# Kernel tuning notes

Hardware: AMD Instinct MI355X
Metric: run time of the kernel (lower is better)

The kernel has to match this reference:

```python
import jax, jax.numpy as jnp
import numpy as np

N_NODES = 100000


def _gcn_conv(x, W, b, src, dst, norm, num_nodes):
    # PyG GCNConv: h = x @ W; out = scatter_add(norm_e * h[src] -> dst) + b
    h = x @ W                               # [N, out]
    msgs = h[src] * norm[:, None]           # [E', out]
    agg = jax.ops.segment_sum(msgs, dst, num_segments=num_nodes)
    return agg + b


def _gcn_norm(edge_index, num_nodes):
    # add self-loops, then sym-normalize: deg^-1/2[src] * deg^-1/2[dst]
    loops = jnp.arange(num_nodes, dtype=edge_index.dtype)
    src = jnp.concatenate([edge_index[0], loops])
    dst = jnp.concatenate([edge_index[1], loops])
    deg = jax.ops.segment_sum(jnp.ones_like(dst, dtype=jnp.float32), dst,
                              num_segments=num_nodes)
    dis = jnp.where(deg > 0, jax.lax.rsqrt(jnp.maximum(deg, 1.0)), 0.0)
    norm = dis[src] * dis[dst]              # [E + N]
    return src, dst, norm


def setup_inputs() -> dict:
    key = jax.random.key(0)
    k1, k2, k3, k4 = jax.random.split(key, 4)
    in_feat, hidden, n_classes = 512, 16, 16
    n_edges = 3200000
    x = jax.random.normal(k1, (N_NODES, in_feat), dtype=jnp.float32)
    edge_index = jax.random.randint(k2, (2, n_edges), 0, N_NODES, dtype=jnp.int64)
    W1 = jax.random.normal(k3, (in_feat, hidden), dtype=jnp.float32) / np.sqrt(in_feat)
    b1 = jnp.zeros((hidden,), dtype=jnp.float32)
    W2 = jax.random.normal(k4, (hidden, n_classes), dtype=jnp.float32) / np.sqrt(hidden)
    b2 = jnp.zeros((n_classes,), dtype=jnp.float32)
    return {"x": x, "edge_index": edge_index, "W1": W1, "b1": b1, "W2": W2, "b2": b2}


def reference(x, edge_index, W1, b1, W2, b2):
    num_nodes = x.shape[0]
    src, dst, norm = _gcn_norm(edge_index, num_nodes)
    h = _gcn_conv(x, W1, b1, src, dst, norm, num_nodes)
    h = jax.nn.relu(h)
    # dropout is identity at inference (training=False)
    h = _gcn_conv(h, W2, b2, src, dst, norm, num_nodes)
    return jax.nn.log_softmax(h, axis=1)
```

## Files before the change

### kernel.cpp

```cpp
#include <hip/hip_runtime.h>
#include <hip/hip_bf16.h>
#include <math.h>

#define NNODES 100000
#define NBUCK 8
#define XRANGE 12500
#define NCHUNK 32
#define CAP 408192
#define BCHUNK 3125
#define GT64 1563

typedef __attribute__((ext_vector_type(8))) short bf16x8;
typedef __attribute__((ext_vector_type(4))) float f32x4;

__device__ __forceinline__ float bflo(unsigned int u) {
  union { unsigned int i; float f; } v; v.i = u << 16; return v.f;
}
__device__ __forceinline__ float bfhi(unsigned int u) {
  union { unsigned int i; float f; } v; v.i = u & 0xFFFF0000u; return v.f;
}
__device__ __forceinline__ unsigned int f2bf1(float f) {
  union { float f; unsigned int i; } v; v.f = f;
  return (v.i + 0x7FFFu + ((v.i >> 16) & 1u)) >> 16;
}
__device__ __forceinline__ unsigned int f2bf2(float a, float b) {
  return f2bf1(a) | (f2bf1(b) << 16);
}

__device__ __forceinline__ int edge_val(const void* eidx, int is64, size_t i) {
  if (is64) return (int)((const long long*)eidx)[i];
  return ((const int*)eidx)[i];
}

__device__ __forceinline__ bf16x8 cvt8(const float4& p, const float4& q) {
  union { unsigned int u[4]; bf16x8 v; } r;
  r.u[0] = f2bf2(p.x, p.y);
  r.u[1] = f2bf2(p.z, p.w);
  r.u[2] = f2bf2(q.x, q.y);
  r.u[3] = f2bf2(q.z, q.w);
  return r.v;
}

__device__ __forceinline__ bf16x8 cvtW(const float* wf) {
  union { unsigned int u[4]; bf16x8 v; } r;
  r.u[0] = f2bf2(wf[0], wf[1]);
  r.u[1] = f2bf2(wf[2], wf[3]);
  r.u[2] = f2bf2(wf[4], wf[5]);
  r.u[3] = f2bf2(wf[6], wf[7]);
  return r.v;
}

__global__ void k_init(const void* eidx, int* flag, int* gcur) {
  int t = threadIdx.x;
  int bad = 0;
  const unsigned long long* p = (const unsigned long long*)eidx;
  for (int i = t; i < 1024; i += 64)
    if (p[i] >> 32) bad = 1;
  unsigned long long b = __ballot(bad);
  if (t == 0) flag[0] = (b == 0ULL) ? 1 : 0;
  if (t < NBUCK) gcur[t] = 0;
}

__global__ void k_binmm(const void* eidx, const int* __restrict__ flag, int* gcur,
                        int* __restrict__ sArr, unsigned short* __restrict__ dArr,
                        int E, int binBlocks,
                        const float* __restrict__ x, const float* __restrict__ W,
                        unsigned short* __restrict__ gb, int gemmBlocks) {
  __shared__ unsigned int s_sb[BCHUNK];
  __shared__ unsigned short s_dl[BCHUNK];
  __shared__ int bbase[NBUCK], lcur[NBUCK], wcnt[4][NBUCK];

  int grp = blockIdx.x / 11, role = blockIdx.x % 11;
  if (role < 3) {
    int gid = grp * 3 + role;
    if (gid >= gemmBlocks) return;
    int wid = threadIdx.x >> 6;
    int tile = gid * 4 + wid;
    if (tile >= GT64) return;
    int lane = threadIdx.x & 63;
    int row0 = tile * 64;
    int q8 = lane >> 4;
    int jm = lane & 15;
    const float4* x4 = (const float4*)x;
    size_t xb0 = (size_t)min(row0 + jm,      NNODES - 1) * 128 + q8 * 2;
    size_t xb1 = (size_t)min(row0 + 16 + jm, NNODES - 1) * 128 + q8 * 2;
    size_t xb2 = (size_t)min(row0 + 32 + jm, NNODES - 1) * 128 + q8 * 2;
    size_t xb3 = (size_t)min(row0 + 48 + jm, NNODES - 1) * 128 + q8 * 2;

    f32x4 acc0 = {0.f, 0.f, 0.f, 0.f}, acc1 = {0.f, 0.f, 0.f, 0.f};
    f32x4 acc2 = {0.f, 0.f, 0.f, 0.f}, acc3 = {0.f, 0.f, 0.f, 0.f};
    #pragma unroll
    for (int kc = 0; kc < 16; ++kc) {
      float4 va0 = x4[xb0 + kc * 8], va1 = x4[xb0 + kc * 8 + 1];
      float4 vb0 = x4[xb1 + kc * 8], vb1 = x4[xb1 + kc * 8 + 1];
      float4 vc0 = x4[xb2 + kc * 8], vc1 = x4[xb2 + kc * 8 + 1];
      float4 vd0 = x4[xb3 + kc * 8], vd1 = x4[xb3 + kc * 8 + 1];
      float wf[8];
      #pragma unroll
      for (int i = 0; i < 8; ++i)
        wf[i] = W[(size_t)(kc * 32 + q8 * 8 + i) * 16 + jm];
      bf16x8 bfr = cvtW(wf);
      acc0 = __builtin_amdgcn_mfma_f32_16x16x32_bf16(cvt8(va0, va1), bfr, acc0, 0, 0, 0);
      acc1 = __builtin_amdgcn_mfma_f32_16x16x32_bf16(cvt8(vb0, vb1), bfr, acc1, 0, 0, 0);
      acc2 = __builtin_amdgcn_mfma_f32_16x16x32_bf16(cvt8(vc0, vc1), bfr, acc2, 0, 0, 0);
      acc3 = __builtin_amdgcn_mfma_f32_16x16x32_bf16(cvt8(vd0, vd1), bfr, acc3, 0, 0, 0);
    }
    #pragma unroll
    for (int r = 0; r < 4; ++r) {
      int rl = q8 * 4 + r;
      int w0 = row0 + rl, w1 = row0 + 16 + rl, w2 = row0 + 32 + rl, w3 = row0 + 48 + rl;
      if (w0 < NNODES) gb[(size_t)w0 * 16 + jm] = (unsigned short)f2bf1(acc0[r]);
      if (w1 < NNODES) gb[(size_t)w1 * 16 + jm] = (unsigned short)f2bf1(acc1[r]);
      if (w2 < NNODES) gb[(size_t)w2 * 16 + jm] = (unsigned short)f2bf1(acc2[r]);
      if (w3 < NNODES) gb[(size_t)w3 * 16 + jm] = (unsigned short)f2bf1(acc3[r]);
    }
    return;
  }

  int bid = grp * 8 + (role - 3);
  if (bid >= binBlocks) return;
  int is64 = flag[0];
  int beg = bid * BCHUNK;
  int end = min(beg + BCHUNK, E);
  int cnt = end - beg;
  int lane = threadIdx.x & 63, wid = threadIdx.x >> 6;

  int cl = 0;
  for (int i = threadIdx.x; i < cnt; i += 256) {
    int e = beg + i;
    int s = edge_val(eidx, is64, e);
    int d = edge_val(eidx, is64, (size_t)E + e);
    int bk = d / XRANGE;
    s_sb[i] = (unsigned int)s | ((unsigned int)bk << 17);
    s_dl[i] = (unsigned short)(d - bk * XRANGE);
    #pragma unroll
    for (int b = 0; b < NBUCK; ++b) {
      unsigned long long m = __ballot(bk == b);
      if (lane == b) cl += __popcll(m);
    }
  }
  if (lane < NBUCK) wcnt[wid][lane] = cl;
  __syncthreads();
  if (threadIdx.x < NBUCK) {
    int t = wcnt[0][threadIdx.x] + wcnt[1][threadIdx.x] +
            wcnt[2][threadIdx.x] + wcnt[3][threadIdx.x];
    bbase[threadIdx.x] = atomicAdd(&gcur[threadIdx.x], t);
    lcur[threadIdx.x] = 0;
  }
  __syncthreads();

  for (int i = threadIdx.x; i < cnt; i += 256) {
    unsigned int sb = s_sb[i];
    int bk = (int)(sb >> 17);
    int s = (int)(sb & 0x1FFFFu);
    unsigned short dl = s_dl[i];
    #pragma unroll
    for (int b = 0; b < NBUCK; ++b) {
      unsigned long long m = __ballot(bk == b);
      int c = __popcll(m);
      if (!c) continue;
      int leader = __ffsll((unsigned long long)m) - 1;
      int base = 0;
      if (lane == leader) base = atomicAdd(&lcur[b], c);
      base = __shfl(base, leader);
      if (bk == b) {
        int rank = __popcll(m & ((1ULL << lane) - 1));
        int gpos = bbase[b] + base + rank;
        if (gpos < CAP) {
          sArr[(size_t)b * CAP + gpos] = s;
          dArr[(size_t)b * CAP + gpos] = dl;
        }
      }
    }
  }
}

__global__ void k_hist(const int* __restrict__ gcur, const unsigned short* __restrict__ dArr,
                       int* __restrict__ cntc) {
  int b = blockIdx.x & (NBUCK - 1);
  int c = blockIdx.x >> 3;
  __shared__ int h[XRANGE];
  for (int i = threadIdx.x; i < XRANGE; i += 256) h[i] = 0;
  __syncthreads();
  int nE = min(gcur[b], CAP);
  int ce = (nE + NCHUNK - 1) / NCHUNK;
  int beg = c * ce, end = min(beg + ce, nE);
  const unsigned short* dp = dArr + (size_t)b * CAP;
  for (int e = beg + threadIdx.x; e < end; e += 256)
    atomicAdd(&h[dp[e]], 1);
  __syncthreads();
  int lo = b * XRANGE;
  for (int i = threadIdx.x; i < XRANGE; i += 256)
    cntc[(size_t)c * NNODES + lo + i] = h[i];
}

__global__ void k_dis(const int* __restrict__ cntc, int* __restrict__ tot,
                      float* __restrict__ dis, int* __restrict__ bsum,
                      unsigned int* __restrict__ gb1, int n) {
  int i = blockIdx.x * 256 + threadIdx.x;
  int t = 0;
  if (i < n) {
    #pragma unroll
    for (int c = 0; c < NCHUNK; ++c) t += cntc[(size_t)c * NNODES + i];
    tot[i] = t;
    float dd = rsqrtf((float)(t + 1));
    dis[i] = dd;
    uint4* g4 = (uint4*)gb1;
    uint4 pa = g4[(size_t)i * 2], pb = g4[(size_t)i * 2 + 1];
    pa.x = f2bf2(bflo(pa.x) * dd, bfhi(pa.x) * dd);
    pa.y = f2bf2(bflo(pa.y) * dd, bfhi(pa.y) * dd);
    pa.z = f2bf2(bflo(pa.z) * dd, bfhi(pa.z) * dd);
    pa.w = f2bf2(bflo(pa.w) * dd, bfhi(pa.w) * dd);
    pb.x = f2bf2(bflo(pb.x) * dd, bfhi(pb.x) * dd);
    pb.y = f2bf2(bflo(pb.y) * dd, bfhi(pb.y) * dd);
    pb.z = f2bf2(bflo(pb.z) * dd, bfhi(pb.z) * dd);
    pb.w = f2bf2(bflo(pb.w) * dd, bfhi(pb.w) * dd);
    g4[(size_t)i * 2] = pa;
    g4[(size_t)i * 2 + 1] = pb;
  }
  int v = t;
  #pragma unroll
  for (int d = 32; d > 0; d >>= 1) v += __shfl_down(v, d);
  __shared__ int ws4[4];
  if ((threadIdx.x & 63) == 0) ws4[threadIdx.x >> 6] = v;
  __syncthreads();
  if (threadIdx.x == 0) bsum[blockIdx.x] = ws4[0] + ws4[1] + ws4[2] + ws4[3];
}

__global__ void k_scan_fc(const int* __restrict__ tot, const int* __restrict__ bsum,
                          int* __restrict__ rowptr, int* __restrict__ cntc, int n, int nb) {
  __shared__ int ps[512];
  __shared__ int s[256];
  int t = threadIdx.x;
  ps[t] = (t < nb) ? bsum[t] : 0;
  ps[t + 256] = (t + 256 < nb) ? bsum[t + 256] : 0;
  __syncthreads();
  for (int d = 1; d < 512; d <<= 1) {
    int u0 = (t >= d) ? ps[t - d] : 0;
    int u1 = (t + 256 >= d) ? ps[t + 256 - d] : 0;
    __syncthreads();
    ps[t] += u0;
    ps[t + 256] += u1;
    __syncthreads();
  }
  int bex = (blockIdx.x == 0) ? 0 : ps[blockIdx.x - 1];
  if (blockIdx.x == 0 && t == 0) rowptr[n] = ps[nb - 1];

  int idx = blockIdx.x * 256 + t;
  int v = (idx < n) ? tot[idx] : 0;
  s[t] = v;
  __syncthreads();
  for (int d = 1; d < 256; d <<= 1) {
    int u = (t >= d) ? s[t - d] : 0;
    __syncthreads();
    s[t] += u;
    __syncthreads();
  }
  if (idx < n) {
    int run = bex + s[t] - v;
    rowptr[idx] = run;
    #pragma unroll
    for (int c = 0; c < NCHUNK; ++c) {
      size_t id2 = (size_t)c * NNODES + idx;
      int tc = cntc[id2];
      cntc[id2] = run;
      run += tc;
    }
  }
}

__global__ void k_scatter(const int* __restrict__ gcur, const int* __restrict__ sArr,
                          const unsigned short* __restrict__ dArr,
                          const int* __restrict__ cntc, int* __restrict__ col) {
  int b = blockIdx.x & (NBUCK - 1);
  int c = blockIdx.x >> 3;
  __shared__ int cur[XRANGE];
  int lo = b * XRANGE;
  for (int i = threadIdx.x; i < XRANGE; i += 256)
    cur[i] = cntc[(size_t)c * NNODES + lo + i];
  __syncthreads();
  int nE = min(gcur[b], CAP);
  int ce = (nE + NCHUNK - 1) / NCHUNK;
  int beg = c * ce, end = min(beg + ce, nE);
  const int* sp = sArr + (size_t)b * CAP;
  const unsigned short* dp = dArr + (size_t)b * CAP;
  for (int e = beg + threadIdx.x; e < end; e += 256) {
    int d = dp[e];
    int pos = atomicAdd(&cur[d], 1);
    col[pos] = sp[e];
  }
}

__global__ void k_gemm2(const float* __restrict__ o1, const float* __restrict__ W,
                        const float* __restrict__ dis, unsigned int* __restrict__ gb, int nrows) {
  int row = blockIdx.x * blockDim.x + threadIdx.x;
  if (row >= nrows) return;
  const float4* xr = (const float4*)(o1 + (size_t)row * 16);
  float4 x0 = xr[0], x1 = xr[1], x2 = xr[2], x3 = xr[3];
  float xv[16] = {x0.x, x0.y, x0.z, x0.w, x1.x, x1.y, x1.z, x1.w,
                  x2.x, x2.y, x2.z, x2.w, x3.x, x3.y, x3.z, x3.w};
  float acc[16];
  #pragma unroll
  for (int j = 0; j < 16; ++j) acc[j] = 0.f;
  #pragma unroll
  for (int k = 0; k < 16; ++k) {
    const float* wr = W + (size_t)k * 16;
    #pragma unroll
    for (int j = 0; j < 16; ++j)
      acc[j] = fmaf(xv[k], wr[j], acc[j]);
  }
  float dd = dis[row];
  uint4 pa, pb;
  pa.x = f2bf2(acc[0] * dd, acc[1] * dd);
  pa.y = f2bf2(acc[2] * dd, acc[3] * dd);
  pa.z = f2bf2(acc[4] * dd, acc[5] * dd);
  pa.w = f2bf2(acc[6] * dd, acc[7] * dd);
  pb.x = f2bf2(acc[8] * dd, acc[9] * dd);
  pb.y = f2bf2(acc[10] * dd, acc[11] * dd);
  pb.z = f2bf2(acc[12] * dd, acc[13] * dd);
  pb.w = f2bf2(acc[14] * dd, acc[15] * dd);
  uint4* g4 = (uint4*)gb;
  g4[(size_t)row * 2] = pa;
  g4[(size_t)row * 2 + 1] = pb;
}

__device__ __forceinline__ void gather8v2(const uint4* gp, const int* __restrict__ col,
                                          int beg, int end, int h, int slot, float* acc) {
  #pragma unroll
  for (int j = 0; j < 8; ++j) acc[j] = 0.f;
  for (int e = beg + slot; e < end; e += 16) {
    int s = col[e];
    uint4 v = gp[(size_t)s * 2 + h];
    acc[0] += bflo(v.x); acc[1] += bfhi(v.x);
    acc[2] += bflo(v.y); acc[3] += bfhi(v.y);
    acc[4] += bflo(v.z); acc[5] += bfhi(v.z);
    acc[6] += bflo(v.w); acc[7] += bfhi(v.w);
  }
  #pragma unroll
  for (int d = 2; d < 32; d <<= 1) {
    #pragma unroll
    for (int j = 0; j < 8; ++j) acc[j] += __shfl_xor(acc[j], d);
  }
}

__global__ void k_agg1(const unsigned int* __restrict__ gb, const int* __restrict__ col,
                       const int* __restrict__ rowptr, const float* __restrict__ dis,
                       const float* __restrict__ bias, float* __restrict__ o1) {
  int wid = threadIdx.x >> 6;
  int lane = threadIdx.x & 63;
  int n2 = lane >> 5;
  int node = blockIdx.x * 8 + wid * 2 + n2;
  if (node >= NNODES) return;
  int rem = lane & 31;
  int h = rem & 1, slot = rem >> 1;
  const uint4* gp = (const uint4*)gb;
  float acc[8];
  gather8v2(gp, col, rowptr[node], rowptr[node + 1], h, slot, acc);
  uint4 sv = gp[(size_t)node * 2 + h];
  acc[0] += bflo(sv.x); acc[1] += bfhi(sv.x);
  acc[2] += bflo(sv.y); acc[3] += bfhi(sv.y);
  acc[4] += bflo(sv.z); acc[5] += bfhi(sv.z);
  acc[6] += bflo(sv.w); acc[7] += bfhi(sv.w);
  float dd = dis[node];
  const float4* b4 = (const float4*)bias;
  float4 ba = b4[2 * h], bb = b4[2 * h + 1];
  float z0 = fmaxf(fmaf(dd, acc[0], ba.x), 0.f);
  float z1 = fmaxf(fmaf(dd, acc[1], ba.y), 0.f);
  float z2 = fmaxf(fmaf(dd, acc[2], ba.z), 0.f);
  float z3 = fmaxf(fmaf(dd, acc[3], ba.w), 0.f);
  float z4 = fmaxf(fmaf(dd, acc[4], bb.x), 0.f);
  float z5 = fmaxf(fmaf(dd, acc[5], bb.y), 0.f);
  float z6 = fmaxf(fmaf(dd, acc[6], bb.z), 0.f);
  float z7 = fmaxf(fmaf(dd, acc[7], bb.w), 0.f);
  if (slot == 0) {
    float4* o4 = (float4*)o1;
    o4[(size_t)node * 4 + 2 * h] = make_float4(z0, z1, z2, z3);
    o4[(size_t)node * 4 + 2 * h + 1] = make_float4(z4, z5, z6, z7);
  }
}

__global__ void k_agg2(const unsigned int* __restrict__ gb, const int* __restrict__ col,
                       const int* __restrict__ rowptr, const float* __restrict__ dis,
                       const float* __restrict__ bias, float* __restrict__ out) {
  int wid = threadIdx.x >> 6;
  int lane = threadIdx.x & 63;
  int n2 = lane >> 5;
  int node = blockIdx.x * 8 + wid * 2 + n2;
  if (node >= NNODES) return;
  int rem = lane & 31;
  int h = rem & 1, slot = rem >> 1;
  const uint4* gp = (const uint4*)gb;
  float acc[8];
  gather8v2(gp, col, rowptr[node], rowptr[node + 1], h, slot, acc);
  uint4 sv = gp[(size_t)node * 2 + h];
  acc[0] += bflo(sv.x); acc[1] += bfhi(sv.x);
  acc[2] += bflo(sv.y); acc[3] += bfhi(sv.y);
  acc[4] += bflo(sv.z); acc[5] += bfhi(sv.z);
  acc[6] += bflo(sv.w); acc[7] += bfhi(sv.w);
  float dd = dis[node];
  const float4* b4 = (const float4*)bias;
  float4 ba = b4[2 * h], bb = b4[2 * h + 1];
  float z[8];
  z[0] = fmaf(dd, acc[0], ba.x); z[1] = fmaf(dd, acc[1], ba.y);
  z[2] = fmaf(dd, acc[2], ba.z); z[3] = fmaf(dd, acc[3], ba.w);
  z[4] = fmaf(dd, acc[4], bb.x); z[5] = fmaf(dd, acc[5], bb.y);
  z[6] = fmaf(dd, acc[6], bb.z); z[7] = fmaf(dd, acc[7], bb.w);
  float m = z[0];
  #pragma unroll
  for (int j = 1; j < 8; ++j) m = fmaxf(m, z[j]);
  m = fmaxf(m, __shfl_xor(m, 1));
  float se = 0.f;
  #pragma unroll
  for (int j = 0; j < 8; ++j) se += expf(z[j] - m);
  se += __shfl_xor(se, 1);
  float lg = m + logf(se);
  if (slot == 0) {
    float4* o4 = (float4*)out;
    o4[(size_t)node * 4 + 2 * h] = make_float4(z[0] - lg, z[1] - lg, z[2] - lg, z[3] - lg);
    o4[(size_t)node * 4 + 2 * h + 1] = make_float4(z[4] - lg, z[5] - lg, z[6] - lg, z[7] - lg);
  }
}

extern "C" void kernel_launch(void* const* d_in, const int* in_sizes, int n_in,
                              void* d_out, int out_size, void* d_ws, size_t ws_size,
                              hipStream_t stream) {
  const float* x  = (const float*)d_in[0];
  const void*  ei = d_in[1];
  const float* W1 = (const float*)d_in[2];
  const float* b1 = (const float*)d_in[3];
  const float* W2 = (const float*)d_in[4];
  const float* b2 = (const float*)d_in[5];
  float* out = (float*)d_out;

  const int n = NNODES;
  const int E = in_sizes[1] / 2;

  char* ws = (char*)d_ws;
  size_t off = 0;
  auto alloc = [&](size_t bytes) -> void* {
    void* p = ws + off;
    off = (off + bytes + 255) & ~(size_t)255;
    return p;
  };
  int*            flag   = (int*)            alloc(256);
  int*            gcur   = (int*)            alloc(256);
  int*            sArr   = (int*)            alloc((size_t)NBUCK * CAP * 4);
  unsigned short* dArr   = (unsigned short*) alloc((size_t)NBUCK * CAP * 2);
  int*            cntc   = (int*)            alloc((size_t)NCHUNK * n * 4);
  int*            tot    = (int*)            alloc((size_t)n * 4);
  float*          dis    = (float*)          alloc((size_t)n * 4);
  int*            rowptr = (int*)            alloc((size_t)(n + 1) * 4);
  int*            bsum   = (int*)            alloc(4096);
  int*            col    = (int*)            alloc((size_t)E * 4);
  unsigned short* gb1    = (unsigned short*) alloc((size_t)n * 16 * 2);
  float*          o1  = (float*)sArr;
  unsigned int*   gb2 = (unsigned int*)dArr;
  (void)ws_size; (void)n_in; (void)out_size;

  int nb = (n + 255) / 256;
  int binBlocks  = (E + BCHUNK - 1) / BCHUNK;
  int gemmBlocks = (GT64 + 3) / 4;
  int groups = max((gemmBlocks + 2) / 3, (binBlocks + 7) / 8);
  int grid = groups * 11;

  k_init<<<1, 64, 0, stream>>>(ei, flag, gcur);
  k_binmm<<<grid, 256, 0, stream>>>(ei, flag, gcur, sArr, dArr, E, binBlocks,
                                    x, W1, gb1, gemmBlocks);
  k_hist<<<NBUCK * NCHUNK, 256, 0, stream>>>(gcur, dArr, cntc);
  k_dis<<<nb, 256, 0, stream>>>(cntc, tot, dis, bsum, (unsigned int*)gb1, n);
  k_scan_fc<<<nb, 256, 0, stream>>>(tot, bsum, rowptr, cntc, n, nb);
  k_scatter<<<NBUCK * NCHUNK, 256, 0, stream>>>(gcur, sArr, dArr, cntc, col);

  k_agg1<<<(n + 7) / 8, 256, 0, stream>>>((const unsigned int*)gb1, col, rowptr, dis, b1, o1);
  k_gemm2<<<(n + 255) / 256, 256, 0, stream>>>(o1, W2, dis, (unsigned int*)gb2, n);
  k_agg2<<<(n + 7) / 8, 256, 0, stream>>>(gb2, col, rowptr, dis, b2, out);
}
```

Measured before the change: 198.5 us.

## Spread first-layer GEMM tiles across binning, histogram, degree and scan kernels

```diff
diff --git a/kernel.cpp b/kernel.cpp
--- a/kernel.cpp
+++ b/kernel.cpp
@@ -48,6 +48,50 @@
   r.u[2] = f2bf2(wf[4], wf[5]);
   r.u[3] = f2bf2(wf[6], wf[7]);
   return r.v;
+}
+
+__device__ __forceinline__ void gemm_tile64(const float* __restrict__ x,
+                                            const float* __restrict__ W,
+                                            unsigned short* __restrict__ gb,
+                                            int tile) {
+  if (tile >= GT64) return;
+  int lane = threadIdx.x & 63;
+  int row0 = tile * 64;
+  int q8 = lane >> 4;
+  int jm = lane & 15;
+  const float4* x4 = (const float4*)x;
+  size_t xb0 = (size_t)min(row0 + jm,      NNODES - 1) * 128 + q8 * 2;
+  size_t xb1 = (size_t)min(row0 + 16 + jm, NNODES - 1) * 128 + q8 * 2;
+  size_t xb2 = (size_t)min(row0 + 32 + jm, NNODES - 1) * 128 + q8 * 2;
+  size_t xb3 = (size_t)min(row0 + 48 + jm, NNODES - 1) * 128 + q8 * 2;
+
+  f32x4 acc0 = {0.f, 0.f, 0.f, 0.f}, acc1 = {0.f, 0.f, 0.f, 0.f};
+  f32x4 acc2 = {0.f, 0.f, 0.f, 0.f}, acc3 = {0.f, 0.f, 0.f, 0.f};
+  #pragma unroll
+  for (int kc = 0; kc < 16; ++kc) {
+    float4 va0 = x4[xb0 + kc * 8], va1 = x4[xb0 + kc * 8 + 1];
+    float4 vb0 = x4[xb1 + kc * 8], vb1 = x4[xb1 + kc * 8 + 1];
+    float4 vc0 = x4[xb2 + kc * 8], vc1 = x4[xb2 + kc * 8 + 1];
+    float4 vd0 = x4[xb3 + kc * 8], vd1 = x4[xb3 + kc * 8 + 1];
+    float wf[8];
+    #pragma unroll
+    for (int i = 0; i < 8; ++i)
+      wf[i] = W[(size_t)(kc * 32 + q8 * 8 + i) * 16 + jm];
+    bf16x8 bfr = cvtW(wf);
+    acc0 = __builtin_amdgcn_mfma_f32_16x16x32_bf16(cvt8(va0, va1), bfr, acc0, 0, 0, 0);
+    acc1 = __builtin_amdgcn_mfma_f32_16x16x32_bf16(cvt8(vb0, vb1), bfr, acc1, 0, 0, 0);
+    acc2 = __builtin_amdgcn_mfma_f32_16x16x32_bf16(cvt8(vc0, vc1), bfr, acc2, 0, 0, 0);
+    acc3 = __builtin_amdgcn_mfma_f32_16x16x32_bf16(cvt8(vd0, vd1), bfr, acc3, 0, 0, 0);
+  }
+  #pragma unroll
+  for (int r = 0; r < 4; ++r) {
+    int rl = q8 * 4 + r;
+    int w0 = row0 + rl, w1 = row0 + 16 + rl, w2 = row0 + 32 + rl, w3 = row0 + 48 + rl;
+    if (w0 < NNODES) gb[(size_t)w0 * 16 + jm] = (unsigned short)f2bf1(acc0[r]);
+    if (w1 < NNODES) gb[(size_t)w1 * 16 + jm] = (unsigned short)f2bf1(acc1[r]);
+    if (w2 < NNODES) gb[(size_t)w2 * 16 + jm] = (unsigned short)f2bf1(acc2[r]);
+    if (w3 < NNODES) gb[(size_t)w3 * 16 + jm] = (unsigned short)f2bf1(acc3[r]);
+  }
 }
 
 __global__ void k_init(const void* eidx, int* flag, int* gcur) {
@@ -65,59 +109,18 @@
                         int* __restrict__ sArr, unsigned short* __restrict__ dArr,
                         int E, int binBlocks,
                         const float* __restrict__ x, const float* __restrict__ W,
-                        unsigned short* __restrict__ gb, int gemmBlocks) {
+                        unsigned short* __restrict__ gb, int gBase, int gBlocks) {
   __shared__ unsigned int s_sb[BCHUNK];
   __shared__ unsigned short s_dl[BCHUNK];
   __shared__ int bbase[NBUCK], lcur[NBUCK], wcnt[4][NBUCK];
 
   int grp = blockIdx.x / 11, role = blockIdx.x % 11;
-  if (role < 3) {
-    int gid = grp * 3 + role;
-    if (gid >= gemmBlocks) return;
-    int wid = threadIdx.x >> 6;
-    int tile = gid * 4 + wid;
-    if (tile >= GT64) return;
-    int lane = threadIdx.x & 63;
-    int row0 = tile * 64;
-    int q8 = lane >> 4;
-    int jm = lane & 15;
-    const float4* x4 = (const float4*)x;
-    size_t xb0 = (size_t)min(row0 + jm,      NNODES - 1) * 128 + q8 * 2;
-    size_t xb1 = (size_t)min(row0 + 16 + jm, NNODES - 1) * 128 + q8 * 2;
-    size_t xb2 = (size_t)min(row0 + 32 + jm, NNODES - 1) * 128 + q8 * 2;
-    size_t xb3 = (size_t)min(row0 + 48 + jm, NNODES - 1) * 128 + q8 * 2;
-
-    f32x4 acc0 = {0.f, 0.f, 0.f, 0.f}, acc1 = {0.f, 0.f, 0.f, 0.f};
-    f32x4 acc2 = {0.f, 0.f, 0.f, 0.f}, acc3 = {0.f, 0.f, 0.f, 0.f};
-    #pragma unroll
-    for (int kc = 0; kc < 16; ++kc) {
-      float4 va0 = x4[xb0 + kc * 8], va1 = x4[xb0 + kc * 8 + 1];
-      float4 vb0 = x4[xb1 + kc * 8], vb1 = x4[xb1 + kc * 8 + 1];
-      float4 vc0 = x4[xb2 + kc * 8], vc1 = x4[xb2 + kc * 8 + 1];
-      float4 vd0 = x4[xb3 + kc * 8], vd1 = x4[xb3 + kc * 8 + 1];
-      float wf[8];
-      #pragma unroll
-      for (int i = 0; i < 8; ++i)
-        wf[i] = W[(size_t)(kc * 32 + q8 * 8 + i) * 16 + jm];
-      bf16x8 bfr = cvtW(wf);
-      acc0 = __builtin_amdgcn_mfma_f32_16x16x32_bf16(cvt8(va0, va1), bfr, acc0, 0, 0, 0);
-      acc1 = __builtin_amdgcn_mfma_f32_16x16x32_bf16(cvt8(vb0, vb1), bfr, acc1, 0, 0, 0);
-      acc2 = __builtin_amdgcn_mfma_f32_16x16x32_bf16(cvt8(vc0, vc1), bfr, acc2, 0, 0, 0);
-      acc3 = __builtin_amdgcn_mfma_f32_16x16x32_bf16(cvt8(vd0, vd1), bfr, acc3, 0, 0, 0);
-    }
-    #pragma unroll
-    for (int r = 0; r < 4; ++r) {
-      int rl = q8 * 4 + r;
-      int w0 = row0 + rl, w1 = row0 + 16 + rl, w2 = row0 + 32 + rl, w3 = row0 + 48 + rl;
-      if (w0 < NNODES) gb[(size_t)w0 * 16 + jm] = (unsigned short)f2bf1(acc0[r]);
-      if (w1 < NNODES) gb[(size_t)w1 * 16 + jm] = (unsigned short)f2bf1(acc1[r]);
-      if (w2 < NNODES) gb[(size_t)w2 * 16 + jm] = (unsigned short)f2bf1(acc2[r]);
-      if (w3 < NNODES) gb[(size_t)w3 * 16 + jm] = (unsigned short)f2bf1(acc3[r]);
-    }
+  if (role == 10) {
+    int gid = grp;
+    if (gid < gBlocks) gemm_tile64(x, W, gb, gBase + gid * 4 + (int)(threadIdx.x >> 6));
     return;
   }
-
-  int bid = grp * 8 + (role - 3);
+  int bid = grp * 10 + role;
   if (bid >= binBlocks) return;
   int is64 = flag[0];
   int beg = bid * BCHUNK;
@@ -176,10 +179,20 @@
 }
 
 __global__ void k_hist(const int* __restrict__ gcur, const unsigned short* __restrict__ dArr,
-                       int* __restrict__ cntc) {
-  int b = blockIdx.x & (NBUCK - 1);
-  int c = blockIdx.x >> 3;
+                       int* __restrict__ cntc,
+                       const float* __restrict__ x, const float* __restrict__ W,
+                       unsigned short* __restrict__ gb, int gBase, int gBlocks) {
   __shared__ int h[XRANGE];
+  int grp = blockIdx.x / 7, role = blockIdx.x % 7;
+  if (role >= 5) {
+    int gid = grp * 2 + (role - 5);
+    if (gid < gBlocks) gemm_tile64(x, W, gb, gBase + gid * 4 + (int)(threadIdx.x >> 6));
+    return;
+  }
+  int hid = grp * 5 + role;
+  if (hid >= NBUCK * NCHUNK) return;
+  int b = hid & (NBUCK - 1);
+  int c = hid >> 3;
   for (int i = threadIdx.x; i < XRANGE; i += 256) h[i] = 0;
   __syncthreads();
   int nE = min(gcur[b], CAP);
@@ -195,28 +208,23 @@
 }
 
 __global__ void k_dis(const int* __restrict__ cntc, int* __restrict__ tot,
-                      float* __restrict__ dis, int* __restrict__ bsum,
-                      unsigned int* __restrict__ gb1, int n) {
-  int i = blockIdx.x * 256 + threadIdx.x;
+                      float* __restrict__ dis, int* __restrict__ bsum, int n,
+                      const float* __restrict__ x, const float* __restrict__ W,
+                      unsigned short* __restrict__ gb, int gBase, int gBlocks) {
+  int grp = blockIdx.x / 5, role = blockIdx.x % 5;
+  if (role == 4) {
+    int gid = grp;
+    if (gid < gBlocks) gemm_tile64(x, W, gb, gBase + gid * 4 + (int)(threadIdx.x >> 6));
+    return;
+  }
+  int bid = grp * 4 + role;
+  int i = bid * 256 + threadIdx.x;
   int t = 0;
   if (i < n) {
     #pragma unroll
     for (int c = 0; c < NCHUNK; ++c) t += cntc[(size_t)c * NNODES + i];
     tot[i] = t;
-    float dd = rsqrtf((float)(t + 1));
-    dis[i] = dd;
-    uint4* g4 = (uint4*)gb1;
-    uint4 pa = g4[(size_t)i * 2], pb = g4[(size_t)i * 2 + 1];
-    pa.x = f2bf2(bflo(pa.x) * dd, bfhi(pa.x) * dd);
-    pa.y = f2bf2(bflo(pa.y) * dd, bfhi(pa.y) * dd);
-    pa.z = f2bf2(bflo(pa.z) * dd, bfhi(pa.z) * dd);
-    pa.w = f2bf2(bflo(pa.w) * dd, bfhi(pa.w) * dd);
-    pb.x = f2bf2(bflo(pb.x) * dd, bfhi(pb.x) * dd);
-    pb.y = f2bf2(bflo(pb.y) * dd, bfhi(pb.y) * dd);
-    pb.z = f2bf2(bflo(pb.z) * dd, bfhi(pb.z) * dd);
-    pb.w = f2bf2(bflo(pb.w) * dd, bfhi(pb.w) * dd);
-    g4[(size_t)i * 2] = pa;
-    g4[(size_t)i * 2 + 1] = pb;
+    dis[i] = rsqrtf((float)(t + 1));
   }
   int v = t;
   #pragma unroll
@@ -224,13 +232,22 @@
   __shared__ int ws4[4];
   if ((threadIdx.x & 63) == 0) ws4[threadIdx.x >> 6] = v;
   __syncthreads();
-  if (threadIdx.x == 0) bsum[blockIdx.x] = ws4[0] + ws4[1] + ws4[2] + ws4[3];
+  if (threadIdx.x == 0 && bid < 1024) bsum[bid] = ws4[0] + ws4[1] + ws4[2] + ws4[3];
 }
 
 __global__ void k_scan_fc(const int* __restrict__ tot, const int* __restrict__ bsum,
-                          int* __restrict__ rowptr, int* __restrict__ cntc, int n, int nb) {
+                          int* __restrict__ rowptr, int* __restrict__ cntc, int n, int nb,
+                          const float* __restrict__ x, const float* __restrict__ W,
+                          unsigned short* __restrict__ gb, int gBase, int gBlocks) {
   __shared__ int ps[512];
   __shared__ int s[256];
+  int grp = blockIdx.x / 11, role = blockIdx.x % 11;
+  if (role >= 9) {
+    int gid = grp * 2 + (role - 9);
+    if (gid < gBlocks) gemm_tile64(x, W, gb, gBase + gid * 4 + (int)(threadIdx.x >> 6));
+    return;
+  }
+  int bid = grp * 9 + role;
   int t = threadIdx.x;
   ps[t] = (t < nb) ? bsum[t] : 0;
   ps[t + 256] = (t + 256 < nb) ? bsum[t + 256] : 0;
@@ -243,10 +260,10 @@
     ps[t + 256] += u1;
     __syncthreads();
   }
-  int bex = (blockIdx.x == 0) ? 0 : ps[blockIdx.x - 1];
-  if (blockIdx.x == 0 && t == 0) rowptr[n] = ps[nb - 1];
-
-  int idx = blockIdx.x * 256 + t;
+  int bex = (bid == 0) ? 0 : ((bid - 1 < 512) ? ps[bid - 1] : 0);
+  if (bid == 0 && t == 0) rowptr[n] = ps[nb - 1];
+
+  int idx = bid * 256 + t;
   int v = (idx < n) ? tot[idx] : 0;
   s[t] = v;
   __syncthreads();
@@ -271,10 +288,32 @@
 
 __global__ void k_scatter(const int* __restrict__ gcur, const int* __restrict__ sArr,
                           const unsigned short* __restrict__ dArr,
-                          const int* __restrict__ cntc, int* __restrict__ col) {
-  int b = blockIdx.x & (NBUCK - 1);
-  int c = blockIdx.x >> 3;
+                          const int* __restrict__ cntc, int* __restrict__ col,
+                          const float* __restrict__ dis, unsigned int* __restrict__ gb1) {
   __shared__ int cur[XRANGE];
+  int grp = blockIdx.x / 5, role = blockIdx.x % 5;
+  if (role == 4) {
+    uint4* g4 = (uint4*)gb1;
+    for (int i = grp * 256 + threadIdx.x; i < NNODES; i += 64 * 256) {
+      float dd = dis[i];
+      uint4 pa = g4[(size_t)i * 2], pb = g4[(size_t)i * 2 + 1];
+      pa.x = f2bf2(bflo(pa.x) * dd, bfhi(pa.x) * dd);
+      pa.y = f2bf2(bflo(pa.y) * dd, bfhi(pa.y) * dd);
+      pa.z = f2bf2(bflo(pa.z) * dd, bfhi(pa.z) * dd);
+      pa.w = f2bf2(bflo(pa.w) * dd, bfhi(pa.w) * dd);
+      pb.x = f2bf2(bflo(pb.x) * dd, bfhi(pb.x) * dd);
+      pb.y = f2bf2(bflo(pb.y) * dd, bfhi(pb.y) * dd);
+      pb.z = f2bf2(bflo(pb.z) * dd, bfhi(pb.z) * dd);
+      pb.w = f2bf2(bflo(pb.w) * dd, bfhi(pb.w) * dd);
+      g4[(size_t)i * 2] = pa;
+      g4[(size_t)i * 2 + 1] = pb;
+    }
+    return;
+  }
+  int sid = grp * 4 + role;
+  if (sid >= NBUCK * NCHUNK) return;
+  int b = sid & (NBUCK - 1);
+  int c = sid >> 3;
   int lo = b * XRANGE;
   for (int i = threadIdx.x; i < XRANGE; i += 256)
     cur[i] = cntc[(size_t)c * NNODES + lo + i];
@@ -458,18 +497,36 @@
   (void)ws_size; (void)n_in; (void)out_size;
 
   int nb = (n + 255) / 256;
-  int binBlocks  = (E + BCHUNK - 1) / BCHUNK;
-  int gemmBlocks = (GT64 + 3) / 4;
-  int groups = max((gemmBlocks + 2) / 3, (binBlocks + 7) / 8);
-  int grid = groups * 11;
+  int binBlocks = (E + BCHUNK - 1) / BCHUNK;
+
+  const int g0 = 103, g1 = 104, g2 = 98, g3 = 86;
+  const int b0 = 0, bsl1 = g0 * 4, bsl2 = (g0 + g1) * 4, bsl3 = (g0 + g1 + g2) * 4;
 
   k_init<<<1, 64, 0, stream>>>(ei, flag, gcur);
-  k_binmm<<<grid, 256, 0, stream>>>(ei, flag, gcur, sArr, dArr, E, binBlocks,
-                                    x, W1, gb1, gemmBlocks);
-  k_hist<<<NBUCK * NCHUNK, 256, 0, stream>>>(gcur, dArr, cntc);
-  k_dis<<<nb, 256, 0, stream>>>(cntc, tot, dis, bsum, (unsigned int*)gb1, n);
-  k_scan_fc<<<nb, 256, 0, stream>>>(tot, bsum, rowptr, cntc, n, nb);
-  k_scatter<<<NBUCK * NCHUNK, 256, 0, stream>>>(gcur, sArr, dArr, cntc, col);
+
+  {
+    int groups = max((binBlocks + 9) / 10, g0);
+    k_binmm<<<groups * 11, 256, 0, stream>>>(ei, flag, gcur, sArr, dArr, E, binBlocks,
+                                             x, W1, gb1, b0, g0);
+  }
+  {
+    int groups = max((NBUCK * NCHUNK + 4) / 5, (g1 + 1) / 2);
+    k_hist<<<groups * 7, 256, 0, stream>>>(gcur, dArr, cntc, x, W1, gb1, bsl1, g1);
+  }
+  {
+    int groups = max((nb + 3) / 4, g2);
+    k_dis<<<groups * 5, 256, 0, stream>>>(cntc, tot, dis, bsum, n, x, W1, gb1, bsl2, g2);
+  }
+  {
+    int groups = max((nb + 8) / 9, (g3 + 1) / 2);
+    k_scan_fc<<<groups * 11, 256, 0, stream>>>(tot, bsum, rowptr, cntc, n, nb,
+                                               x, W1, gb1, bsl3, g3);
+  }
+  {
+    int groups = (NBUCK * NCHUNK) / 4;
+    k_scatter<<<groups * 5, 256, 0, stream>>>(gcur, sArr, dArr, cntc, col, dis,
+                                              (unsigned int*)gb1);
+  }
 
   k_agg1<<<(n + 7) / 8, 256, 0, stream>>>((const unsigned int*)gb1, col, rowptr, dis, b1, o1);
   k_gemm2<<<(n + 255) / 256, 256, 0, stream>>>(o1, W2, dis, (unsigned int*)gb2, n);
```

New measurement: 298.3 us. 50.3% more time.
